# Performance work log

Hardware: AMD Instinct MI355X
Metric: run time of the kernel (lower is better)

The kernel has to match this reference:

```python
import jax, jax.numpy as jnp
from jax import lax
import numpy as np

B, IN, OUT = 32768, 512, 512


def _bit_length(a):
    # a: nonnegative int32. Smear high bit down, then popcount == bit length.
    y = a
    y = y | (y >> 1)
    y = y | (y >> 2)
    y = y | (y >> 4)
    y = y | (y >> 8)
    y = y | (y >> 16)
    return lax.population_count(y)


def trunc_top_bits(v, k=4):
    # compress_top4(|a|,|b|,4): keep top-k significant bits of each magnitude.
    a = jnp.abs(v)
    shift = jnp.maximum(_bit_length(a) - k, 0)
    t = (a >> shift) << shift
    return t * jnp.sign(v)


def setup_inputs() -> dict:
    key = jax.random.key(0)
    k1, k2, k3 = jax.random.split(key, 3)
    bound = 1.0 / np.sqrt(IN)  # matches kaiming_uniform(a=sqrt(5)) + bias bound
    x = jax.random.normal(k1, (B, IN), dtype=jnp.float32)
    weight = jax.random.uniform(k2, (OUT, IN), dtype=jnp.float32, minval=-bound, maxval=bound)
    bias = jax.random.uniform(k3, (OUT,), dtype=jnp.float32, minval=-bound, maxval=bound)
    return {"x": x, "weight": weight, "bias": bias, "weight_sf": 8, "act_sf": 6}


def reference(x, weight, bias, weight_sf, act_sf):
    # Fixed-point quantization: input / 2^{-sf} then trunc-toward-zero int cast
    xi = (x * (2.0 ** act_sf)).astype(jnp.int32)       # [B, IN]
    wi = (weight * (2.0 ** weight_sf)).astype(jnp.int32)  # [OUT, IN]
    # sign/abs decomposition + top-4-bit truncated multiply-accumulate:
    # sum_y compress_top4(|xi|,|wi|) * sign(xi)*sign(wi) == dot of signed truncs
    tx = trunc_top_bits(xi).astype(jnp.float32)
    tw = trunc_top_bits(wi).astype(jnp.float32)
    acc = jnp.einsum("bi,oi->bo", tx, tw)             # [B, OUT], exact in fp32
    scale = (2.0 ** (-act_sf)) * (2.0 ** (-weight_sf))
    return acc * scale + bias[None, :]
```

## Files before the change

### kernel.cpp

```cpp
#include <hip/hip_runtime.h>
#include <stdint.h>

#define B_DIM 32768
#define IN_DIM 512
#define OUT_DIM 512

typedef float f32x4 __attribute__((ext_vector_type(4)));

__device__ __forceinline__ float trunc4(float x, float s) {
    uint32_t u = __float_as_uint(truncf(x * s));
    return __uint_as_float(u & 0xFFF00000u);
}

__global__ void quant_fp8(const float* __restrict__ in, uint32_t* __restrict__ out,
                          int n4, const int* __restrict__ sf) {
    int i = blockIdx.x * blockDim.x + threadIdx.x;
    if (i >= n4) return;
    float scale = (float)(1 << *sf);
    float4 v = ((const float4*)in)[i];
    int p = 0;
    p = __builtin_amdgcn_cvt_pk_fp8_f32(trunc4(v.x, scale), trunc4(v.y, scale), p, false);
    p = __builtin_amdgcn_cvt_pk_fp8_f32(trunc4(v.z, scale), trunc4(v.w, scale), p, true);
    out[i] = (uint32_t)p;
}

__global__ __launch_bounds__(256, 4)
void gemm_f8(const uint8_t* __restrict__ A, const uint8_t* __restrict__ W,
             const float* __restrict__ bias, float* __restrict__ C,
             const int* __restrict__ wsf, const int* __restrict__ asf) {
    __shared__ uint8_t As[128 * 64];
    __shared__ uint8_t Bs[128 * 64];

    const int t    = threadIdx.x;
    const int w    = t >> 6;
    const int lane = t & 63;

    const int b    = blockIdx.x;
    const int xcd  = b & 7;
    const int slot = b >> 3;
    const int bm   = xcd * 32 + (slot >> 2);
    const int bn   = slot & 3;
    const int row0 = bm * 128;
    const int col0 = bn * 128;
    const int wm   = (w & 1) * 64;
    const int wn   = (w >> 1) * 64;

    const int m_st = t >> 2;
    const int goff = ((2 * (t & 3)) ^ (m_st & 6)) * 8;
    const size_t offA = (size_t)(row0 + m_st) * IN_DIM + goff;
    const size_t offB = (size_t)(col0 + m_st) * IN_DIM + goff;

    f32x4 acc[4][4];
    #pragma unroll
    for (int mt = 0; mt < 4; ++mt)
        #pragma unroll
        for (int nt = 0; nt < 4; ++nt)
            acc[mt][nt] = 0.0f;

    for (int k0 = 0; k0 < IN_DIM; k0 += 64) {
        #pragma unroll
        for (int i = 0; i < 2; ++i) {
            const uint8_t* ga = A + offA + (size_t)i * 64 * IN_DIM + k0;
            uint8_t*       la = As + i * 4096 + w * 1024;
            __builtin_amdgcn_global_load_lds((const __attribute__((address_space(1))) void*)ga,
                                             (__attribute__((address_space(3))) void*)la, 16, 0, 0);
            const uint8_t* gb = W + offB + (size_t)i * 64 * IN_DIM + k0;
            uint8_t*       lb = Bs + i * 4096 + w * 1024;
            __builtin_amdgcn_global_load_lds((const __attribute__((address_space(1))) void*)gb,
                                             (__attribute__((address_space(3))) void*)lb, 16, 0, 0);
        }
        __syncthreads();

        const int q  = lane >> 4;
        const int rl = lane & 15;
        const int sx = rl & 6;
        #pragma unroll
        for (int ks = 0; ks < 2; ++ks) {
            const int c  = ks * 4 + q;
            const int cb = (c ^ sx) * 8;
            long af[4], bfr[4];
            #pragma unroll
            for (int mt = 0; mt < 4; ++mt)
                af[mt] = *(const long*)(As + (wm + mt * 16 + rl) * 64 + cb);
            #pragma unroll
            for (int nt = 0; nt < 4; ++nt)
                bfr[nt] = *(const long*)(Bs + (wn + nt * 16 + rl) * 64 + cb);
            #pragma unroll
            for (int mt = 0; mt < 4; ++mt)
                #pragma unroll
                for (int nt = 0; nt < 4; ++nt)
                    acc[mt][nt] = __builtin_amdgcn_mfma_f32_16x16x32_fp8_fp8(af[mt], bfr[nt], acc[mt][nt], 0, 0, 0);
        }
        __syncthreads();
    }

    const float oscale = ldexpf(1.0f, -(*wsf + *asf));
    const int cl = lane & 15;
    const int rg = (lane >> 4) * 4;
    #pragma unroll
    for (int nt = 0; nt < 4; ++nt) {
        const int col = col0 + wn + nt * 16 + cl;
        const float bv = bias[col];
        #pragma unroll
        for (int mt = 0; mt < 4; ++mt) {
            f32x4 a = acc[mt][nt];
            #pragma unroll
            for (int r = 0; r < 4; ++r) {
                const int row = row0 + wm + mt * 16 + rg + r;
                C[(size_t)row * OUT_DIM + col] = a[r] * oscale + bv;
            }
        }
    }
}

extern "C" void kernel_launch(void* const* d_in, const int* in_sizes, int n_in,
                              void* d_out, int out_size, void* d_ws, size_t ws_size,
                              hipStream_t stream) {
    const float* x    = (const float*)d_in[0];
    const float* wgt  = (const float*)d_in[1];
    const float* bias = (const float*)d_in[2];
    const int*   wsf  = (const int*)d_in[3];
    const int*   asf  = (const int*)d_in[4];

    uint8_t* tx = (uint8_t*)d_ws;
    uint8_t* tw = (uint8_t*)d_ws + (size_t)B_DIM * IN_DIM;

    const int nx4 = B_DIM * IN_DIM / 4;
    const int nw4 = OUT_DIM * IN_DIM / 4;
    quant_fp8<<<(nx4 + 255) / 256, 256, 0, stream>>>(x, (uint32_t*)tx, nx4, asf);
    quant_fp8<<<(nw4 + 255) / 256, 256, 0, stream>>>(wgt, (uint32_t*)tw, nw4, wsf);

    const int grid = (B_DIM / 128) * (OUT_DIM / 128);
    gemm_f8<<<grid, 256, 0, stream>>>(tx, tw, bias, (float*)d_out, wsf, asf);
}
```

Before: 135.1 us.

## Double-buffer GEMM LDS tiles and merge the two quantization launches

The GEMM main loop now keeps two LDS buffers per operand. It issues the global-to-LDS loads for the next K tile before running MFMAs on the current one, and needs only one barrier per iteration instead of two. This is meant to hide global load latency behind compute. The x and weight quantization kernels are merged into one launch to save a kernel launch. LDS use per block doubles to 32KB, which can limit occupancy against the 4-blocks-per-CU launch bound.

```diff
diff --git a/kernel.cpp b/kernel.cpp
--- a/kernel.cpp
+++ b/kernel.cpp
@@ -12,24 +12,34 @@
     return __uint_as_float(u & 0xFFF00000u);
 }
 
-__global__ void quant_fp8(const float* __restrict__ in, uint32_t* __restrict__ out,
-                          int n4, const int* __restrict__ sf) {
+__global__ void quant_fp8_2(const float* __restrict__ x, const float* __restrict__ w,
+                            uint32_t* __restrict__ ox, uint32_t* __restrict__ ow,
+                            int nx4, int nw4,
+                            const int* __restrict__ asf, const int* __restrict__ wsf) {
     int i = blockIdx.x * blockDim.x + threadIdx.x;
-    if (i >= n4) return;
-    float scale = (float)(1 << *sf);
-    float4 v = ((const float4*)in)[i];
+    const float4* in;
+    uint32_t* out;
+    float scale;
+    if (i < nx4) {
+        in = (const float4*)x + i;  out = ox + i;  scale = (float)(1 << *asf);
+    } else {
+        int j = i - nx4;
+        if (j >= nw4) return;
+        in = (const float4*)w + j;  out = ow + j;  scale = (float)(1 << *wsf);
+    }
+    float4 v = *in;
     int p = 0;
     p = __builtin_amdgcn_cvt_pk_fp8_f32(trunc4(v.x, scale), trunc4(v.y, scale), p, false);
     p = __builtin_amdgcn_cvt_pk_fp8_f32(trunc4(v.z, scale), trunc4(v.w, scale), p, true);
-    out[i] = (uint32_t)p;
+    *out = (uint32_t)p;
 }
 
 __global__ __launch_bounds__(256, 4)
 void gemm_f8(const uint8_t* __restrict__ A, const uint8_t* __restrict__ W,
              const float* __restrict__ bias, float* __restrict__ C,
              const int* __restrict__ wsf, const int* __restrict__ asf) {
-    __shared__ uint8_t As[128 * 64];
-    __shared__ uint8_t Bs[128 * 64];
+    __shared__ uint8_t As[2][128 * 64];
+    __shared__ uint8_t Bs[2][128 * 64];
 
     const int t    = threadIdx.x;
     const int w    = t >> 6;
@@ -57,41 +67,71 @@
         for (int nt = 0; nt < 4; ++nt)
             acc[mt][nt] = 0.0f;
 
-    for (int k0 = 0; k0 < IN_DIM; k0 += 64) {
-        #pragma unroll
-        for (int i = 0; i < 2; ++i) {
-            const uint8_t* ga = A + offA + (size_t)i * 64 * IN_DIM + k0;
-            uint8_t*       la = As + i * 4096 + w * 1024;
-            __builtin_amdgcn_global_load_lds((const __attribute__((address_space(1))) void*)ga,
-                                             (__attribute__((address_space(3))) void*)la, 16, 0, 0);
-            const uint8_t* gb = W + offB + (size_t)i * 64 * IN_DIM + k0;
-            uint8_t*       lb = Bs + i * 4096 + w * 1024;
-            __builtin_amdgcn_global_load_lds((const __attribute__((address_space(1))) void*)gb,
-                                             (__attribute__((address_space(3))) void*)lb, 16, 0, 0);
+    #pragma unroll
+    for (int i = 0; i < 2; ++i) {
+        const uint8_t* ga = A + offA + (size_t)i * 64 * IN_DIM;
+        uint8_t*       la = &As[0][i * 4096 + w * 1024];
+        __builtin_amdgcn_global_load_lds((const __attribute__((address_space(1))) void*)ga,
+                                         (__attribute__((address_space(3))) void*)la, 16, 0, 0);
+        const uint8_t* gb = W + offB + (size_t)i * 64 * IN_DIM;
+        uint8_t*       lb = &Bs[0][i * 4096 + w * 1024];
+        __builtin_amdgcn_global_load_lds((const __attribute__((address_space(1))) void*)gb,
+                                         (__attribute__((address_space(3))) void*)lb, 16, 0, 0);
+    }
+    asm volatile("s_waitcnt vmcnt(0) lgkmcnt(0)" ::: "memory");
+    __builtin_amdgcn_sched_barrier(0);
+    __builtin_amdgcn_s_barrier();
+    __builtin_amdgcn_sched_barrier(0);
+
+    #pragma unroll
+    for (int k = 0; k < 8; ++k) {
+        const int cur = k & 1;
+        const int nxt = cur ^ 1;
+
+        if (k < 7) {
+            #pragma unroll
+            for (int i = 0; i < 2; ++i) {
+                const uint8_t* ga = A + offA + (size_t)i * 64 * IN_DIM + (k + 1) * 64;
+                uint8_t*       la = &As[nxt][i * 4096 + w * 1024];
+                __builtin_amdgcn_global_load_lds((const __attribute__((address_space(1))) void*)ga,
+                                                 (__attribute__((address_space(3))) void*)la, 16, 0, 0);
+                const uint8_t* gb = W + offB + (size_t)i * 64 * IN_DIM + (k + 1) * 64;
+                uint8_t*       lb = &Bs[nxt][i * 4096 + w * 1024];
+                __builtin_amdgcn_global_load_lds((const __attribute__((address_space(1))) void*)gb,
+                                                 (__attribute__((address_space(3))) void*)lb, 16, 0, 0);
+            }
         }
-        __syncthreads();
+        __builtin_amdgcn_sched_barrier(0);
 
-        const int q  = lane >> 4;
-        const int rl = lane & 15;
-        const int sx = rl & 6;
-        #pragma unroll
-        for (int ks = 0; ks < 2; ++ks) {
-            const int c  = ks * 4 + q;
-            const int cb = (c ^ sx) * 8;
-            long af[4], bfr[4];
+        {
+            const int q  = lane >> 4;
+            const int rl = lane & 15;
+            const int sx = rl & 6;
             #pragma unroll
-            for (int mt = 0; mt < 4; ++mt)
-                af[mt] = *(const long*)(As + (wm + mt * 16 + rl) * 64 + cb);
-            #pragma unroll
-            for (int nt = 0; nt < 4; ++nt)
-                bfr[nt] = *(const long*)(Bs + (wn + nt * 16 + rl) * 64 + cb);
-            #pragma unroll
-            for (int mt = 0; mt < 4; ++mt)
+            for (int ks = 0; ks < 2; ++ks) {
+                const int c  = ks * 4 + q;
+                const int cb = (c ^ sx) * 8;
+                long af[4], bfr[4];
+                #pragma unroll
+                for (int mt = 0; mt < 4; ++mt)
+                    af[mt] = *(const long*)(&As[cur][0] + (wm + mt * 16 + rl) * 64 + cb);
                 #pragma unroll
                 for (int nt = 0; nt < 4; ++nt)
-                    acc[mt][nt] = __builtin_amdgcn_mfma_f32_16x16x32_fp8_fp8(af[mt], bfr[nt], acc[mt][nt], 0, 0, 0);
+                    bfr[nt] = *(const long*)(&Bs[cur][0] + (wn + nt * 16 + rl) * 64 + cb);
+                #pragma unroll
+                for (int mt = 0; mt < 4; ++mt)
+                    #pragma unroll
+                    for (int nt = 0; nt < 4; ++nt)
+                        acc[mt][nt] = __builtin_amdgcn_mfma_f32_16x16x32_fp8_fp8(af[mt], bfr[nt], acc[mt][nt], 0, 0, 0);
+            }
         }
-        __syncthreads();
+
+        if (k < 7) {
+            asm volatile("s_waitcnt vmcnt(0) lgkmcnt(0)" ::: "memory");
+            __builtin_amdgcn_sched_barrier(0);
+            __builtin_amdgcn_s_barrier();
+            __builtin_amdgcn_sched_barrier(0);
+        }
     }
 
     const float oscale = ldexpf(1.0f, -(*wsf + *asf));
@@ -127,8 +167,8 @@
 
     const int nx4 = B_DIM * IN_DIM / 4;
     const int nw4 = OUT_DIM * IN_DIM / 4;
-    quant_fp8<<<(nx4 + 255) / 256, 256, 0, stream>>>(x, (uint32_t*)tx, nx4, asf);
-    quant_fp8<<<(nw4 + 255) / 256, 256, 0, stream>>>(wgt, (uint32_t*)tw, nw4, wsf);
+    quant_fp8_2<<<(nx4 + nw4 + 255) / 256, 256, 0, stream>>>(
+        x, wgt, (uint32_t*)tx, (uint32_t*)tw, nx4, nw4, asf, wsf);
 
     const int grid = (B_DIM / 128) * (OUT_DIM / 128);
     gemm_f8<<<grid, 256, 0, stream>>>(tx, tw, bias, (float*)d_out, wsf, asf);
```

New measurement: 131.9 us. 2.4% less time.
